# Kernel tuning notes

Hardware: AMD Instinct MI355X
Metric: run time of the kernel (lower is better)

## Reference

```python
import jax, jax.numpy as jnp
import numpy as np

B, T, H, IN, OUT = 128, 256, 1024, 1, 1


def setup_inputs() -> dict:
    key = jax.random.key(0)
    ks = jax.random.split(key, 11)
    s = 1.0 / np.sqrt(H)
    u = lambda k, shape: jax.random.uniform(k, shape, jnp.float32, -s, s)
    return {
        "input_X": jax.random.normal(ks[0], (B, T), jnp.float32),
        "W_ih0": u(ks[1], (4 * H, IN)),
        "W_hh0": u(ks[2], (4 * H, H)),
        "b_ih0": u(ks[3], (4 * H,)),
        "b_hh0": u(ks[4], (4 * H,)),
        "W_ih1": u(ks[5], (4 * H, H)),
        "W_hh1": u(ks[6], (4 * H, H)),
        "b_ih1": u(ks[7], (4 * H,)),
        "b_hh1": u(ks[8], (4 * H,)),
        "W_lin": u(ks[9], (OUT, H)),
        "b_lin": u(ks[10], (OUT,)),
        "future": 0,
    }


def _lstm_cell(x, h, c, W_ih, W_hh, b_ih, b_hh):
    # gates: [B, 4H], PyTorch LSTMCell gate order: i, f, g, o
    gates = x @ W_ih.T + b_ih + h @ W_hh.T + b_hh
    i, f, g, o = jnp.split(gates, 4, axis=-1)
    c_new = jax.nn.sigmoid(f) * c + jax.nn.sigmoid(i) * jnp.tanh(g)
    h_new = jax.nn.sigmoid(o) * jnp.tanh(c_new)
    return h_new, c_new


def reference(input_X, W_ih0, W_hh0, b_ih0, b_hh0, W_ih1, W_hh1, b_ih1, b_hh1,
              W_lin, b_lin, future):
    batch = input_X.shape[0]
    h0 = jnp.zeros((batch, H), input_X.dtype)
    c0 = jnp.zeros((batch, H), input_X.dtype)
    h1 = jnp.zeros((batch, H), input_X.dtype)
    c1 = jnp.zeros((batch, H), input_X.dtype)

    def step(carry, x_t):  # x_t: [B, 1]
        h0, c0, h1, c1 = carry
        h0, c0 = _lstm_cell(x_t, h0, c0, W_ih0, W_hh0, b_ih0, b_hh0)
        h1, c1 = _lstm_cell(h0, h1, c1, W_ih1, W_hh1, b_ih1, b_hh1)
        y = h1 @ W_lin.T + b_lin  # [B, OUT]
        return (h0, c0, h1, c1), y

    xs = input_X.T[:, :, None]  # [T, B, 1]
    carry, ys = jax.lax.scan(step, (h0, c0, h1, c1), xs)
    outputs = jnp.transpose(ys, (1, 0, 2))  # [B, T, OUT]

    y = ys[-1]
    fut = []
    for _ in range(int(future)):
        carry, y = step(carry, y)
        fut.append(y)
    if fut:
        outputs = jnp.concatenate([outputs, jnp.stack(fut, axis=1)], axis=1)
    return jnp.squeeze(outputs, axis=2)  # [B, T+future]
```

## Files before the change

### kernel.cpp

```cpp
#include <hip/hip_runtime.h>
#include <stdint.h>

typedef _Float16 f16;
typedef f16 half8 __attribute__((ext_vector_type(8)));
typedef float f32x4 __attribute__((ext_vector_type(4)));

constexpr int HID = 1024;
constexpr int NBAT = 128;
constexpr int SEQ = 256;
constexpr int NL0 = 64;
constexpr int NL1 = 128;
constexpr int NBLK = NL0 + NL1;
constexpr int HROWB = 4096;
constexpr int WROWB0 = 2064;
constexpr int WROWB1 = 4112;
constexpr int ZOFF = 32 * WROWB1;
constexpr int ZBYTES = 4160;
constexpr int WLDS = ZOFF + ZBYTES;
constexpr int LDS_TOTAL = WLDS;

constexpr int SY_INIT = 0;
constexpr int SY_BARG = 32;
constexpr int SY_CNT = 64;
constexpr int SY_BARAX = 64 + 256;

__device__ __forceinline__ float sigm(float x) { return 1.0f / (1.0f + __expf(-x)); }
__device__ __forceinline__ float tanh_(float x) {
  float e = __expf(2.0f * x);
  return (e - 1.0f) / (e + 1.0f);
}
__device__ __forceinline__ void vm0() {
  asm volatile("s_waitcnt vmcnt(0)" ::: "memory");
}
__device__ __forceinline__ void spin_until(int* p, int target) {
  uint64_t t0 = __builtin_amdgcn_s_memtime();
  while (__hip_atomic_load(p, __ATOMIC_RELAXED, __HIP_MEMORY_SCOPE_AGENT) < target) {
    __builtin_amdgcn_s_sleep(1);
    if (__builtin_amdgcn_s_memtime() - t0 > (1ULL << 29)) break;
  }
}

__global__ __launch_bounds__(256, 1) void lstm_persist(
    const float* __restrict__ X,
    const float* __restrict__ Wih0, const float* __restrict__ Whh0,
    const float* __restrict__ bih0, const float* __restrict__ bhh0,
    const float* __restrict__ Wih1, const float* __restrict__ Whh1,
    const float* __restrict__ bih1, const float* __restrict__ bhh1,
    const float* __restrict__ Wlin,
    f16* __restrict__ Hcat,
    float* __restrict__ yp,
    int* __restrict__ sy) {
  extern __shared__ char smem[];
  char* Wl = smem;

  const int bid = blockIdx.x, tid = threadIdx.x;
  const bool isL0 = bid < NL0;
  const int j = isL0 ? bid : bid - NL0;
  const int w = tid >> 6, l = tid & 63;
  const int l15 = l & 15, lhi = l >> 4;

  int xcd;
  asm volatile("s_getreg_b32 %0, hwreg(HW_REG_XCC_ID)" : "=s"(xcd));
  xcd &= 7;

  if (isL0) {
    for (int it = 0; it < 256; ++it) {
      int e = it * 256 + tid;
      int r = e >> 10, k = e & 1023;
      int grow = (r >> 4) * HID + j * 16 + (r & 15);
      *(f16*)(Wl + r * WROWB0 + 2 * k) = (f16)Whh0[(size_t)grow * HID + k];
    }
  } else {
    for (int it = 0; it < 256; ++it) {
      int e = it * 256 + tid;
      int r = e >> 11, k = e & 2047;
      int grow = (r >> 3) * HID + j * 8 + (r & 7);
      float v = (k < 1024) ? Wih1[(size_t)grow * HID + k]
                           : Whh1[(size_t)grow * HID + (k - 1024)];
      *(f16*)(Wl + r * WROWB1 + 2 * k) = (f16)v;
    }
    for (int e = tid; e < ZBYTES / 2; e += 256)
      *(f16*)(Wl + ZOFF + 2 * e) = (f16)0.f;
  }

  float bi, bf, bg, bo, wi_i = 0, wi_f = 0, wi_g = 0, wi_o = 0, wl = 0;
  if (isL0) {
    int m = j * 16 + l15;
    bi = bih0[m] + bhh0[m];
    bf = bih0[HID + m] + bhh0[HID + m];
    bg = bih0[2 * HID + m] + bhh0[2 * HID + m];
    bo = bih0[3 * HID + m] + bhh0[3 * HID + m];
    wi_i = Wih0[m]; wi_f = Wih0[HID + m];
    wi_g = Wih0[2 * HID + m]; wi_o = Wih0[3 * HID + m];
  } else {
    int u = j * 8 + (l15 & 7);
    bi = bih1[u] + bhh1[u];
    bf = bih1[HID + u] + bhh1[HID + u];
    bg = bih1[2 * HID + u] + bhh1[2 * HID + u];
    bo = bih1[3 * HID + u] + bhh1[3 * HID + u];
    wl = (l15 < 8) ? Wlin[u] : 0.f;
  }
  float cst[8];
#pragma unroll
  for (int q = 0; q < 8; ++q) cst[q] = 0.f;

  int cx = 0, nx = 0;
  if (tid == 0) {
    __hip_atomic_fetch_add(&sy[SY_CNT + 32 * xcd], 1, __ATOMIC_RELAXED,
                           __HIP_MEMORY_SCOPE_AGENT);
    __hip_atomic_fetch_add(&sy[SY_INIT], 1, __ATOMIC_RELAXED, __HIP_MEMORY_SCOPE_AGENT);
    spin_until(&sy[SY_INIT], NBLK);
    cx = __hip_atomic_load(&sy[SY_CNT + 32 * xcd], __ATOMIC_RELAXED,
                           __HIP_MEMORY_SCOPE_AGENT);
#pragma unroll
    for (int x = 0; x < 8; ++x)
      nx += (__hip_atomic_load(&sy[SY_CNT + 32 * x], __ATOMIC_RELAXED,
                               __HIP_MEMORY_SCOPE_AGENT) > 0);
  }
  __syncthreads();

  const char* Wb = Wl + l15 * WROWB0 + lhi * 16;
  const char* Wg0 = Wl + ((l15 < 8) ? (0 * 8 + l15) * WROWB1 : ZOFF) + lhi * 16;
  const char* Wg1 = Wl + ((l15 < 8) ? (1 * 8 + l15) * WROWB1 : ZOFF) + lhi * 16;
  const char* Wg2 = Wl + ((l15 < 8) ? (2 * 8 + l15) * WROWB1 : ZOFF) + lhi * 16;
  const char* Wg3 = Wl + ((l15 < 8) ? (3 * 8 + l15) * WROWB1 : ZOFF) + lhi * 16;

  for (int i = 1; i <= SEQ + 1; ++i) {
    const bool active = isL0 ? (i <= SEQ) : (i >= 2);
    if (active) {
      const char* Asrc = (const char*)Hcat + (size_t)((i - 1) & 1) * NBAT * HROWB;
      const char* a0p = Asrc + (size_t)(32 * w + l15) * HROWB + lhi * 16;
      const char* a1p = a0p + (size_t)16 * HROWB;
      f16* Hw = Hcat + (size_t)(i & 1) * NBAT * 2048;

      if (isL0) {
        float xr[8];
#pragma unroll
        for (int mf = 0; mf < 2; ++mf)
#pragma unroll
          for (int r = 0; r < 4; ++r)
            xr[mf * 4 + r] = X[(32 * w + 16 * mf + 4 * lhi + r) * SEQ + (i - 1)];

        half8 pa[8], pb[8];
#pragma unroll
        for (int k0 = 0; k0 < 8; ++k0) {
          pa[k0] = *(const half8*)(a0p + k0 * 64);
          pb[k0] = *(const half8*)(a1p + k0 * 64);
        }
        f32x4 acc[2][4];
#pragma unroll
        for (int mf = 0; mf < 2; ++mf)
#pragma unroll
          for (int n = 0; n < 4; ++n) acc[mf][n] = f32x4{0.f, 0.f, 0.f, 0.f};

#pragma unroll
        for (int ck = 0; ck < 32; ++ck) {
          half8 a0 = pa[ck & 7], a1 = pb[ck & 7];
          if (ck < 24) {
            pa[ck & 7] = *(const half8*)(a0p + (ck + 8) * 64);
            pb[ck & 7] = *(const half8*)(a1p + (ck + 8) * 64);
          }
          half8 b0 = *(const half8*)(Wb + ck * 64);
          half8 b1 = *(const half8*)(Wb + 16 * WROWB0 + ck * 64);
          half8 b2 = *(const half8*)(Wb + 32 * WROWB0 + ck * 64);
          half8 b3 = *(const half8*)(Wb + 48 * WROWB0 + ck * 64);
          acc[0][0] = __builtin_amdgcn_mfma_f32_16x16x32_f16(a0, b0, acc[0][0], 0, 0, 0);
          acc[0][1] = __builtin_amdgcn_mfma_f32_16x16x32_f16(a0, b1, acc[0][1], 0, 0, 0);
          acc[0][2] = __builtin_amdgcn_mfma_f32_16x16x32_f16(a0, b2, acc[0][2], 0, 0, 0);
          acc[0][3] = __builtin_amdgcn_mfma_f32_16x16x32_f16(a0, b3, acc[0][3], 0, 0, 0);
          acc[1][0] = __builtin_amdgcn_mfma_f32_16x16x32_f16(a1, b0, acc[1][0], 0, 0, 0);
          acc[1][1] = __builtin_amdgcn_mfma_f32_16x16x32_f16(a1, b1, acc[1][1], 0, 0, 0);
          acc[1][2] = __builtin_amdgcn_mfma_f32_16x16x32_f16(a1, b2, acc[1][2], 0, 0, 0);
          acc[1][3] = __builtin_amdgcn_mfma_f32_16x16x32_f16(a1, b3, acc[1][3], 0, 0, 0);
        }

#pragma unroll
        for (int mf = 0; mf < 2; ++mf) {
#pragma unroll
          for (int r = 0; r < 4; ++r) {
            int b = 32 * w + 16 * mf + 4 * lhi + r;
            float xv = xr[mf * 4 + r];
            float gi = acc[mf][0][r] + bi + xv * wi_i;
            float gf = acc[mf][1][r] + bf + xv * wi_f;
            float gg = acc[mf][2][r] + bg + xv * wi_g;
            float go = acc[mf][3][r] + bo + xv * wi_o;
            float cn = sigm(gf) * cst[mf * 4 + r] + sigm(gi) * tanh_(gg);
            float hn = sigm(go) * tanh_(cn);
            cst[mf * 4 + r] = cn;
            Hw[(size_t)b * 2048 + j * 16 + l15] = (f16)hn;
          }
        }
      } else {
        half8 pa[8], pb[8];
#pragma unroll
        for (int k0 = 0; k0 < 8; ++k0) {
          pa[k0] = *(const half8*)(a0p + k0 * 64);
          pb[k0] = *(const half8*)(a1p + k0 * 64);
        }
        f32x4 acc[2][4];
#pragma unroll
        for (int mf = 0; mf < 2; ++mf)
#pragma unroll
          for (int n = 0; n < 4; ++n) acc[mf][n] = f32x4{0.f, 0.f, 0.f, 0.f};

#pragma unroll
        for (int ck = 0; ck < 64; ++ck) {
          half8 a0 = pa[ck & 7], a1 = pb[ck & 7];
          if (ck < 56) {
            pa[ck & 7] = *(const half8*)(a0p + (ck + 8) * 64);
            pb[ck & 7] = *(const half8*)(a1p + (ck + 8) * 64);
          }
          half8 b0 = *(const half8*)(Wg0 + ck * 64);
          half8 b1 = *(const half8*)(Wg1 + ck * 64);
          half8 b2 = *(const half8*)(Wg2 + ck * 64);
          half8 b3 = *(const half8*)(Wg3 + ck * 64);
          acc[0][0] = __builtin_amdgcn_mfma_f32_16x16x32_f16(a0, b0, acc[0][0], 0, 0, 0);
          acc[0][1] = __builtin_amdgcn_mfma_f32_16x16x32_f16(a0, b1, acc[0][1], 0, 0, 0);
          acc[0][2] = __builtin_amdgcn_mfma_f32_16x16x32_f16(a0, b2, acc[0][2], 0, 0, 0);
          acc[0][3] = __builtin_amdgcn_mfma_f32_16x16x32_f16(a0, b3, acc[0][3], 0, 0, 0);
          acc[1][0] = __builtin_amdgcn_mfma_f32_16x16x32_f16(a1, b0, acc[1][0], 0, 0, 0);
          acc[1][1] = __builtin_amdgcn_mfma_f32_16x16x32_f16(a1, b1, acc[1][1], 0, 0, 0);
          acc[1][2] = __builtin_amdgcn_mfma_f32_16x16x32_f16(a1, b2, acc[1][2], 0, 0, 0);
          acc[1][3] = __builtin_amdgcn_mfma_f32_16x16x32_f16(a1, b3, acc[1][3], 0, 0, 0);
        }

#pragma unroll
        for (int mf = 0; mf < 2; ++mf) {
#pragma unroll
          for (int r = 0; r < 4; ++r) {
            int b = 32 * w + 16 * mf + 4 * lhi + r;
            float gi = acc[mf][0][r] + bi;
            float gf = acc[mf][1][r] + bf;
            float gg = acc[mf][2][r] + bg;
            float go = acc[mf][3][r] + bo;
            float cn = sigm(gf) * cst[mf * 4 + r] + sigm(gi) * tanh_(gg);
            float hn = sigm(go) * tanh_(cn);
            cst[mf * 4 + r] = cn;
            if (l15 < 8) Hw[(size_t)b * 2048 + 1024 + j * 8 + l15] = (f16)hn;
            float v = hn * wl;
            v += __shfl_xor(v, 1);
            v += __shfl_xor(v, 2);
            v += __shfl_xor(v, 4);
            v += __shfl_xor(v, 8);
            if (l15 == 0)
              yp[(size_t)(i - 2) * NBAT * NL1 + b * NL1 + j] = v;
          }
        }
      }
    }

    if (i <= SEQ) {
      vm0();
      __syncthreads();
      if (tid == 0) {
        int old = __hip_atomic_fetch_add(&sy[SY_BARAX + 32 * xcd], 1, __ATOMIC_RELAXED,
                                         __HIP_MEMORY_SCOPE_AGENT);
        if (old == cx * i - 1) {
          asm volatile("buffer_wbl2 sc1\n\ts_waitcnt vmcnt(0)" ::: "memory");
          asm volatile("buffer_inv sc1\n\ts_waitcnt vmcnt(0)" ::: "memory");
          __hip_atomic_fetch_add(&sy[SY_BARG], 1, __ATOMIC_RELAXED,
                                 __HIP_MEMORY_SCOPE_AGENT);
        }
        asm volatile("buffer_inv\n\ts_waitcnt vmcnt(0)" ::: "memory");
        spin_until(&sy[SY_BARG], nx * i);
      }
      __syncthreads();
    }
  }
}

__global__ __launch_bounds__(256) void zero_ws(f16* Hcat, int* sy) {
  int g = blockIdx.x * 256 + threadIdx.x, gs = gridDim.x * 256;
  for (int idx = g; idx < 2 * NBAT * 2048; idx += gs) Hcat[idx] = (f16)0.f;
  for (int idx = g; idx < 1024; idx += gs) sy[idx] = 0;
}

__global__ __launch_bounds__(256) void final_kernel(const float* __restrict__ yp,
                                                    const float* __restrict__ blin,
                                                    float* __restrict__ out) {
  const int idx = blockIdx.x * blockDim.x + threadIdx.x;
  const int t = idx >> 7, b = idx & 127;
  const float* p = yp + ((size_t)t * NBAT + b) * NL1;
  float s = 0.f;
#pragma unroll
  for (int q = 0; q < NL1; ++q) s += p[q];
  out[b * SEQ + t] = s + blin[0];
}

extern "C" void kernel_launch(void* const* d_in, const int* in_sizes, int n_in,
                              void* d_out, int out_size, void* d_ws, size_t ws_size,
                              hipStream_t stream) {
  const float* X = (const float*)d_in[0];
  const float* Wih0 = (const float*)d_in[1];
  const float* Whh0 = (const float*)d_in[2];
  const float* bih0 = (const float*)d_in[3];
  const float* bhh0 = (const float*)d_in[4];
  const float* Wih1 = (const float*)d_in[5];
  const float* Whh1 = (const float*)d_in[6];
  const float* bih1 = (const float*)d_in[7];
  const float* bhh1 = (const float*)d_in[8];
  const float* Wlin = (const float*)d_in[9];
  const float* blin = (const float*)d_in[10];
  float* out = (float*)d_out;

  char* p = (char*)d_ws;
  f16* Hcat = (f16*)p;    p += (size_t)2 * NBAT * 2048 * 2;
  float* yp = (float*)p;  p += (size_t)SEQ * NBAT * NL1 * 4;
  int* sy = (int*)p;      p += 1024 * 4;

  hipFuncSetAttribute((const void*)lstm_persist,
                      hipFuncAttributeMaxDynamicSharedMemorySize, LDS_TOTAL);

  zero_ws<<<256, 256, 0, stream>>>(Hcat, sy);

  lstm_persist<<<NBLK, 256, LDS_TOTAL, stream>>>(
      X, Wih0, Whh0, bih0, bhh0, Wih1, Whh1, bih1, bhh1, Wlin,
      Hcat, yp, sy);

  final_kernel<<<NBAT, 256, 0, stream>>>(yp, blin, out);
}
```

Baseline: 5.138 ms.

## Use per-step hidden-state slots with atomic 8-byte pushes and drop cache flushes

The hidden state moves from a double buffer to a distinct buffer slot per timestep (258 slots). Each block stages its h outputs in LDS and writes them as coalesced 8-byte atomic exchanges at agent scope. The L2 writeback and invalidate instructions are removed from the per-step grid barrier. Fresh addresses each step plus atomics that bypass the non-coherent caches are meant to keep consumers from reading stale lines without explicit flushes. The cost is a much larger workspace, and correctness now depends on the atomic writes being visible to the plain loads in the next step.

```diff
diff --git a/kernel.cpp b/kernel.cpp
--- a/kernel.cpp
+++ b/kernel.cpp
@@ -4,6 +4,7 @@
 typedef _Float16 f16;
 typedef f16 half8 __attribute__((ext_vector_type(8)));
 typedef float f32x4 __attribute__((ext_vector_type(4)));
+typedef unsigned long long u64;
 
 constexpr int HID = 1024;
 constexpr int NBAT = 128;
@@ -12,12 +13,14 @@
 constexpr int NL1 = 128;
 constexpr int NBLK = NL0 + NL1;
 constexpr int HROWB = 4096;
+constexpr int NSLOT = 258;
+constexpr size_t SLOTE = (size_t)NBAT * 2048;
 constexpr int WROWB0 = 2064;
 constexpr int WROWB1 = 4112;
 constexpr int ZOFF = 32 * WROWB1;
 constexpr int ZBYTES = 4160;
 constexpr int WLDS = ZOFF + ZBYTES;
-constexpr int LDS_TOTAL = WLDS;
+constexpr int LDS_TOTAL = WLDS + 4096;
 
 constexpr int SY_INIT = 0;
 constexpr int SY_BARG = 32;
@@ -31,6 +34,9 @@
 }
 __device__ __forceinline__ void vm0() {
   asm volatile("s_waitcnt vmcnt(0)" ::: "memory");
+}
+__device__ __forceinline__ void push8(void* dst, u64 v) {
+  (void)__hip_atomic_exchange((u64*)dst, v, __ATOMIC_RELAXED, __HIP_MEMORY_SCOPE_AGENT);
 }
 __device__ __forceinline__ void spin_until(int* p, int target) {
   uint64_t t0 = __builtin_amdgcn_s_memtime();
@@ -47,11 +53,12 @@
     const float* __restrict__ Wih1, const float* __restrict__ Whh1,
     const float* __restrict__ bih1, const float* __restrict__ bhh1,
     const float* __restrict__ Wlin,
-    f16* __restrict__ Hcat,
+    f16* __restrict__ Hbuf,
     float* __restrict__ yp,
     int* __restrict__ sy) {
   extern __shared__ char smem[];
   char* Wl = smem;
+  char* Pk = smem + WLDS;
 
   const int bid = blockIdx.x, tid = threadIdx.x;
   const bool isL0 = bid < NL0;
@@ -128,10 +135,10 @@
   for (int i = 1; i <= SEQ + 1; ++i) {
     const bool active = isL0 ? (i <= SEQ) : (i >= 2);
     if (active) {
-      const char* Asrc = (const char*)Hcat + (size_t)((i - 1) & 1) * NBAT * HROWB;
+      const char* Asrc = (const char*)(Hbuf + (size_t)(i - 1) * SLOTE);
+      char* Hw = (char*)(Hbuf + (size_t)i * SLOTE);
       const char* a0p = Asrc + (size_t)(32 * w + l15) * HROWB + lhi * 16;
       const char* a1p = a0p + (size_t)16 * HROWB;
-      f16* Hw = Hcat + (size_t)(i & 1) * NBAT * 2048;
 
       if (isL0) {
         float xr[8];
@@ -178,7 +185,6 @@
         for (int mf = 0; mf < 2; ++mf) {
 #pragma unroll
           for (int r = 0; r < 4; ++r) {
-            int b = 32 * w + 16 * mf + 4 * lhi + r;
             float xv = xr[mf * 4 + r];
             float gi = acc[mf][0][r] + bi + xv * wi_i;
             float gf = acc[mf][1][r] + bf + xv * wi_f;
@@ -187,8 +193,17 @@
             float cn = sigm(gf) * cst[mf * 4 + r] + sigm(gi) * tanh_(gg);
             float hn = sigm(go) * tanh_(cn);
             cst[mf * 4 + r] = cn;
-            Hw[(size_t)b * 2048 + j * 16 + l15] = (f16)hn;
+            *(f16*)(Pk + w * 1024 + (16 * mf + 4 * lhi + r) * 32 + l15 * 2) = (f16)hn;
           }
+        }
+        asm volatile("s_waitcnt lgkmcnt(0)" ::: "memory");
+        {
+          const char* src = Pk + w * 1024 + (l >> 1) * 32 + (l & 1) * 16;
+          u64 v0 = *(const u64*)src;
+          u64 v1 = *(const u64*)(src + 8);
+          char* dst = Hw + (size_t)(32 * w + (l >> 1)) * HROWB + j * 32 + (l & 1) * 16;
+          push8(dst, v0);
+          push8(dst + 8, v1);
         }
       } else {
         half8 pa[8], pb[8];
@@ -236,7 +251,8 @@
             float cn = sigm(gf) * cst[mf * 4 + r] + sigm(gi) * tanh_(gg);
             float hn = sigm(go) * tanh_(cn);
             cst[mf * 4 + r] = cn;
-            if (l15 < 8) Hw[(size_t)b * 2048 + 1024 + j * 8 + l15] = (f16)hn;
+            if (l15 < 8)
+              *(f16*)(Pk + w * 512 + (16 * mf + 4 * lhi + r) * 16 + l15 * 2) = (f16)hn;
             float v = hn * wl;
             v += __shfl_xor(v, 1);
             v += __shfl_xor(v, 2);
@@ -246,6 +262,13 @@
               yp[(size_t)(i - 2) * NBAT * NL1 + b * NL1 + j] = v;
           }
         }
+        asm volatile("s_waitcnt lgkmcnt(0)" ::: "memory");
+        {
+          u64 v = *(const u64*)(Pk + w * 512 + (l >> 1) * 16 + (l & 1) * 8);
+          char* dst =
+              Hw + (size_t)(32 * w + (l >> 1)) * HROWB + 2048 + j * 16 + (l & 1) * 8;
+          push8(dst, v);
+        }
       }
     }
 
@@ -255,13 +278,9 @@
       if (tid == 0) {
         int old = __hip_atomic_fetch_add(&sy[SY_BARAX + 32 * xcd], 1, __ATOMIC_RELAXED,
                                          __HIP_MEMORY_SCOPE_AGENT);
-        if (old == cx * i - 1) {
-          asm volatile("buffer_wbl2 sc1\n\ts_waitcnt vmcnt(0)" ::: "memory");
-          asm volatile("buffer_inv sc1\n\ts_waitcnt vmcnt(0)" ::: "memory");
+        if (old == cx * i - 1)
           __hip_atomic_fetch_add(&sy[SY_BARG], 1, __ATOMIC_RELAXED,
                                  __HIP_MEMORY_SCOPE_AGENT);
-        }
-        asm volatile("buffer_inv\n\ts_waitcnt vmcnt(0)" ::: "memory");
         spin_until(&sy[SY_BARG], nx * i);
       }
       __syncthreads();
@@ -269,9 +288,9 @@
   }
 }
 
-__global__ __launch_bounds__(256) void zero_ws(f16* Hcat, int* sy) {
+__global__ __launch_bounds__(256) void zero_ws(f16* Hbuf, int* sy) {
   int g = blockIdx.x * 256 + threadIdx.x, gs = gridDim.x * 256;
-  for (int idx = g; idx < 2 * NBAT * 2048; idx += gs) Hcat[idx] = (f16)0.f;
+  for (size_t idx = g; idx < 2 * SLOTE; idx += gs) Hbuf[idx] = (f16)0.f;
   for (int idx = g; idx < 1024; idx += gs) sy[idx] = 0;
 }
 
@@ -304,18 +323,18 @@
   float* out = (float*)d_out;
 
   char* p = (char*)d_ws;
-  f16* Hcat = (f16*)p;    p += (size_t)2 * NBAT * 2048 * 2;
+  f16* Hbuf = (f16*)p;    p += (size_t)NSLOT * SLOTE * 2;
   float* yp = (float*)p;  p += (size_t)SEQ * NBAT * NL1 * 4;
   int* sy = (int*)p;      p += 1024 * 4;
 
   hipFuncSetAttribute((const void*)lstm_persist,
                       hipFuncAttributeMaxDynamicSharedMemorySize, LDS_TOTAL);
 
-  zero_ws<<<256, 256, 0, stream>>>(Hcat, sy);
+  zero_ws<<<256, 256, 0, stream>>>(Hbuf, sy);
 
   lstm_persist<<<NBLK, 256, LDS_TOTAL, stream>>>(
       X, Wih0, Whh0, bih0, bhh0, Wih1, Whh1, bih1, bhh1, Wlin,
-      Hcat, yp, sy);
+      Hbuf, yp, sy);
 
   final_kernel<<<NBAT, 256, 0, stream>>>(yp, blin, out);
 }
```

Measured after the change: 4.890 ms. 1.05x faster.
